# Kernel optimization log

Measured on AMD Instinct MI355X. Metric: run time of the kernel, lower is better.

## Reference

```python
import jax, jax.numpy as jnp
import numpy as np

TOPK_FRAC = 0.05  # init arg `topk` (fraction of pool kept)


def setup_inputs() -> dict:
    key = jax.random.key(0)
    k1, k2 = jax.random.split(key)
    x = jax.random.normal(k1, (16, 256, 32, 32), dtype=jnp.float32)
    # nn.Parameter(torch.rand(P, C)) -> uniform [0, 1)
    visual_concept_pool = jax.random.uniform(k2, (2048, 256), dtype=jnp.float32)
    return {"x": x, "visual_concept_pool": visual_concept_pool}


def reference(x, visual_concept_pool):
    n, c, h, w = x.shape
    P = visual_concept_pool.shape[0]
    L = h * w
    xf = x.reshape(n, c, L)                              # [n, c, L]
    # dot_product[n, P, L] = pool @ xf
    dot = jnp.einsum('pc,ncl->npl', visual_concept_pool, xf)
    pool_norm = jnp.sqrt(jnp.sum(visual_concept_pool ** 2, axis=1))   # [P]
    x_norm = jnp.sqrt(jnp.sum(xf ** 2, axis=1))                        # [n, L]
    cos = dot / (pool_norm[None, :, None] * x_norm[:, None, :])       # [n, P, L]

    # mode 1.1: top-k over the pool dimension per (n, pixel)
    keep = int(TOPK_FRAC * P)
    cos_t = jnp.transpose(cos, (0, 2, 1))                # [n, L, P]
    _, idx = jax.lax.top_k(jnp.abs(cos_t), keep)         # [n, L, keep]
    mask = jnp.zeros_like(cos_t).at[
        jnp.arange(n)[:, None, None],
        jnp.arange(L)[None, :, None],
        idx,
    ].set(1.0)                                           # [n, L, P]
    masked = cos_t * mask
    normed = masked / jnp.sum(masked, axis=-1, keepdims=True)  # renormalize over P
    # reconstruct[n, c, L] = pool^T @ cos
    recon = jnp.einsum('pc,nlp->ncl', visual_concept_pool, normed)
    return recon.reshape(n, c, h, w)
```

## Files before the change

### kernel.cpp

```cpp
#include <hip/hip_runtime.h>
#include <hip/hip_fp16.h>

typedef unsigned short u16;
typedef _Float16 half8 __attribute__((ext_vector_type(8)));
typedef float floatx4 __attribute__((ext_vector_type(4)));

#define C_DIM 256
#define P_DIM 2048
#define L_DIM 1024
#define N_DIM 16
#define KEEP 102
#define KPAD 104
#define QTR_PIX 4096
#define SCALE 256.0f

__device__ __forceinline__ void st8(u16* dst, const u16* s) {
  uint4 u;
  u.x = (unsigned)s[0] | ((unsigned)s[1] << 16);
  u.y = (unsigned)s[2] | ((unsigned)s[3] << 16);
  u.z = (unsigned)s[4] | ((unsigned)s[5] << 16);
  u.w = (unsigned)s[6] | ((unsigned)s[7] << 16);
  *(uint4*)dst = u;
}

__device__ __forceinline__ u16 f2h_ftz(float v) {
  if (fabsf(v) < 6.103515625e-5f) return 0;
  return __half_as_ushort(__float2half(v));
}

__device__ __forceinline__ void gl_lds16(const u16* g, u16* l) {
  __builtin_amdgcn_global_load_lds(
      (const __attribute__((address_space(1))) unsigned int*)g,
      (__attribute__((address_space(3))) unsigned int*)l, 16, 0, 0);
}

union SMem {
  u16 sB[2][2][8][512];
  struct { float tbuf[8][260]; int2 kpw[8][KPAD]; } sel;
};

__global__ __launch_bounds__(256) void k_pinv(const float* __restrict__ pool,
                                              float* __restrict__ pinv) {
  int p = blockIdx.x * 256 + threadIdx.x;
  const float4* row = (const float4*)(pool + (size_t)p * C_DIM);
  float s = 0.f;
#pragma unroll
  for (int i = 0; i < C_DIM / 4; ++i) {
    float4 v = row[i];
    s += v.x * v.x + v.y * v.y + v.z * v.z + v.w * v.w;
  }
  pinv[p] = 1.0f / sqrtf(s);
}

__global__ __launch_bounds__(256) void k_packpool(const float* __restrict__ pool,
                                                  const float* __restrict__ pinv,
                                                  u16* __restrict__ ah,
                                                  u16* __restrict__ al,
                                                  u16* __restrict__ ph) {
  int tid = blockIdx.x * 256 + threadIdx.x;
  int lane = tid & 63;
  int ks = (tid >> 6) & 7;
  int pm = tid >> 9;
  int p = pm * 16 + (lane & 15);
  int c0 = ks * 32 + ((lane >> 4) << 3);
  float sc = pinv[p] * SCALE;
  const float* src = pool + (size_t)p * C_DIM + c0;
  u16 h8[8], l8[8], p8[8];
#pragma unroll
  for (int j = 0; j < 8; ++j) {
    float raw = src[j];
    p8[j] = __half_as_ushort(__float2half(raw));
    float v = raw * sc;
    u16 h = f2h_ftz(v);
    float r = v - __half2float(__ushort_as_half(h));
    h8[j] = h;
    l8[j] = f2h_ftz(r);
  }
  size_t o = (size_t)tid * 8;
  st8(ah + o, h8); st8(al + o, l8);
  st8(ph + (size_t)p * C_DIM + c0, p8);
}

__global__ __launch_bounds__(256) void k_packx(const float* __restrict__ x,
                                               u16* __restrict__ xh,
                                               u16* __restrict__ xl) {
  int tid = blockIdx.x * 256 + threadIdx.x;
  int lane = tid & 63;
  int ks = (tid >> 6) & 7;
  int pn = tid >> 9;
  int pix = pn * 16 + (lane & 15);
  int n = pix >> 10, l = pix & 1023;
  int c0 = ks * 32 + ((lane >> 4) << 3);
  const float* src = x + ((size_t)(n * C_DIM + c0)) * L_DIM + l;
  u16 h8[8], l8[8];
#pragma unroll
  for (int j = 0; j < 8; ++j) {
    float v = src[(size_t)j * L_DIM] * SCALE;
    u16 h = f2h_ftz(v);
    float r = v - __half2float(__ushort_as_half(h));
    h8[j] = h;
    l8[j] = f2h_ftz(r);
  }
  size_t o = (size_t)tid * 8;
  st8(xh + o, h8); st8(xl + o, l8);
}

__device__ __forceinline__ void mfma_body(int b, int mq,
                                          const u16* __restrict__ ah_,
                                          const u16* __restrict__ al_,
                                          const u16* __restrict__ xh_,
                                          const u16* __restrict__ xl_,
                                          float* __restrict__ sbuf,
                                          u16 (*sB)[2][8][512]) {
  const int t = threadIdx.x, lane = t & 63, w = t >> 6;
  const int pT = b & 15, pixT = b >> 4;
  const int pm = pT * 8 + w;
  const int pnBase = mq * 256 + pixT * 8;
  const half8* A8h = (const half8*)ah_;
  const half8* A8l = (const half8*)al_;
  const u16* xsrc[2] = {xh_, xl_};

  floatx4 acc[8];
#pragma unroll
  for (int nt = 0; nt < 8; ++nt) acc[nt] = (floatx4){0.f, 0.f, 0.f, 0.f};

#pragma unroll
  for (int q = 0; q < 2; ++q) {
    int id = w * 2 + q;
    int arr = id >> 3, nt = id & 7;
    gl_lds16(xsrc[arr] + ((size_t)(pnBase + nt) * 512 + lane) * 8,
             &sB[0][arr][nt][0]);
  }
  __syncthreads();

#pragma unroll 1
  for (int ks = 0; ks < 8; ++ks) {
    const int cur = ks & 1;
    half8 aH, aL;
    {
      size_t idx = (size_t)pm * 512 + (size_t)ks * 64 + lane;
      aH = A8h[idx]; aL = A8l[idx];
    }
    if (ks < 7) {
#pragma unroll
      for (int q = 0; q < 2; ++q) {
        int id = w * 2 + q;
        int arr = id >> 3, nt = id & 7;
        gl_lds16(xsrc[arr] + ((size_t)(pnBase + nt) * 512 + (ks + 1) * 64 + lane) * 8,
                 &sB[cur ^ 1][arr][nt][0]);
      }
    }
#pragma unroll
    for (int nt = 0; nt < 8; ++nt) {
      half8 bh = *(const half8*)&sB[cur][0][nt][lane * 8];
      half8 bl = *(const half8*)&sB[cur][1][nt][lane * 8];
      floatx4 c = acc[nt];
      c = __builtin_amdgcn_mfma_f32_16x16x32_f16(aH, bh, c, 0, 0, 0);
      c = __builtin_amdgcn_mfma_f32_16x16x32_f16(aH, bl, c, 0, 0, 0);
      c = __builtin_amdgcn_mfma_f32_16x16x32_f16(aL, bh, c, 0, 0, 0);
      acc[nt] = c;
    }
    __syncthreads();
  }

  const int qr = lane >> 4, cl = lane & 15;
  const int pix0 = pixT * 128;
  const int pcol = pT * 128 + w * 16;
#pragma unroll
  for (int nt = 0; nt < 8; ++nt) {
    float* dst = sbuf + (size_t)(pix0 + nt * 16 + cl) * P_DIM + pcol + qr * 4;
    *(float4*)dst = make_float4(acc[nt][0], acc[nt][1], acc[nt][2], acc[nt][3]);
  }
}

__device__ __forceinline__ void select_body(int b, int sq,
                                            const float* __restrict__ sbuf,
                                            const u16* __restrict__ pool_h,
                                            float* __restrict__ out,
                                            float (*tbuf)[260],
                                            int2 (*kpw)[KPAD]) {
  const int t = threadIdx.x;
  const int lane = t & 63;
  const int wv = t >> 6;
  const int gp0 = sq * QTR_PIX + b * 8;
  const int n = gp0 >> 10;
  const int l0 = gp0 & 1023;
  const float* sp = sbuf + (size_t)(b * 8 + wv) * P_DIM;

  float4 v[8];
#pragma unroll
  for (int q = 0; q < 8; ++q) v[q] = *(const float4*)(sp + q * 256 + lane * 4);

  if (lane < KPAD - KEEP) kpw[wv][KEEP + lane] = make_int2(0, 0);

  float M = 0.f;
#pragma unroll
  for (int q = 0; q < 8; ++q) {
    M = fmaxf(M, fabsf(v[q].x)); M = fmaxf(M, fabsf(v[q].y));
    M = fmaxf(M, fabsf(v[q].z)); M = fmaxf(M, fabsf(v[q].w));
  }
#pragma unroll
  for (int off = 1; off < 64; off <<= 1) M = fmaxf(M, __shfl_xor(M, off));
  const unsigned bitsM = __float_as_uint(M);

  unsigned lo = 0u, hi = bitsM + 1u;
  unsigned m = (bitsM > (5u << 23)) ? (bitsM - (5u << 23)) : ((lo + hi) >> 1);
  while (hi - lo > 1u) {
    float mf = __uint_as_float(m);
    unsigned cnt = 0;
#pragma unroll
    for (int q = 0; q < 8; ++q) {
      cnt += (unsigned)__popcll(__ballot(fabsf(v[q].x) >= mf));
      cnt += (unsigned)__popcll(__ballot(fabsf(v[q].y) >= mf));
      cnt += (unsigned)__popcll(__ballot(fabsf(v[q].z) >= mf));
      cnt += (unsigned)__popcll(__ballot(fabsf(v[q].w) >= mf));
    }
    if (cnt >= KEEP) lo = m; else hi = m;
    m = lo + ((hi - lo) >> 1);
  }
  const float V = __uint_as_float(lo);
  const float Vp = __uint_as_float(lo + 1u);

  unsigned gt = 0;
#pragma unroll
  for (int q = 0; q < 8; ++q) {
    gt += (unsigned)__popcll(__ballot(fabsf(v[q].x) >= Vp));
    gt += (unsigned)__popcll(__ballot(fabsf(v[q].y) >= Vp));
    gt += (unsigned)__popcll(__ballot(fabsf(v[q].z) >= Vp));
    gt += (unsigned)__popcll(__ballot(fabsf(v[q].w) >= Vp));
  }
  const unsigned rrem = (unsigned)KEEP - gt;

  unsigned gmask[8], tmask[8];
#pragma unroll
  for (int q = 0; q < 8; ++q) {
    const float* f = (const float*)&v[q];
    unsigned gm = 0, tm = 0;
#pragma unroll
    for (int rr = 0; rr < 4; ++rr) {
      float av = fabsf(f[rr]);
      if (av >= Vp) gm |= (1u << rr);
      else if (av >= V) tm |= (1u << rr);
    }
    gmask[q] = gm; tmask[q] = tm;
  }

  const unsigned long long lowm = (1ull << lane) - 1ull;
  unsigned base = 0, tiebase = 0;
  float Ssum = 0.f;
#pragma unroll
  for (int q = 0; q < 8; ++q) {
    const float* f = (const float*)&v[q];
    unsigned teq = 0, myeqb = 0;
#pragma unroll
    for (int rr = 0; rr < 4; ++rr) {
      unsigned long long beq = __ballot((tmask[q] >> rr) & 1u);
      teq += (unsigned)__popcll(beq);
      myeqb += (unsigned)__popcll(beq & lowm);
    }
    unsigned km = gmask[q];
    {
      unsigned cum = 0;
#pragma unroll
      for (int rr = 0; rr < 4; ++rr) {
        if ((tmask[q] >> rr) & 1u) {
          if (tiebase + myeqb + cum < rrem) km |= (1u << rr);
          ++cum;
        }
      }
    }
    unsigned long long bk[4];
    unsigned tot = 0, myb = 0;
#pragma unroll
    for (int rr = 0; rr < 4; ++rr) {
      bk[rr] = __ballot((km >> rr) & 1u);
      tot += (unsigned)__popcll(bk[rr]);
      myb += (unsigned)__popcll(bk[rr] & lowm);
    }
    {
      unsigned cum = 0;
#pragma unroll
      for (int rr = 0; rr < 4; ++rr) {
        if ((km >> rr) & 1u) {
          unsigned pos = base + myb + cum;
          kpw[wv][pos] = make_int2(q * 256 + lane * 4 + rr, __float_as_int(f[rr]));
          Ssum += f[rr];
          ++cum;
        }
      }
    }
    base += tot;
    tiebase += teq;
  }

#pragma unroll
  for (int off = 1; off < 64; off <<= 1) Ssum += __shfl_xor(Ssum, off);
  const float invS = 1.0f / Ssum;

  __builtin_amdgcn_wave_barrier();

  float a0 = 0.f, a1 = 0.f, a2 = 0.f, a3 = 0.f;
  const u16* pb = pool_h + 4 * lane;
  int2 e[4];
  uint2 r[4];
#pragma unroll
  for (int j = 0; j < 4; ++j) e[j] = kpw[wv][j];
#pragma unroll
  for (int j = 0; j < 4; ++j) r[j] = *(const uint2*)(pb + (size_t)e[j].x * C_DIM);
  for (int k = 0; k < KPAD; k += 4) {
    int kn = (k + 4 < KPAD) ? k + 4 : 0;
    int2 en[4];
    uint2 rn[4];
#pragma unroll
    for (int j = 0; j < 4; ++j) en[j] = kpw[wv][kn + j];
#pragma unroll
    for (int j = 0; j < 4; ++j) rn[j] = *(const uint2*)(pb + (size_t)en[j].x * C_DIM);
#pragma unroll
    for (int j = 0; j < 4; ++j) {
      float w2 = __int_as_float(e[j].y);
      unsigned rx = r[j].x, ry = r[j].y;
      asm volatile("v_fma_mix_f32 %0, %1, %2, %0 op_sel:[0,0,0] op_sel_hi:[0,1,0]"
                   : "+v"(a0) : "v"(w2), "v"(rx));
      asm volatile("v_fma_mix_f32 %0, %1, %2, %0 op_sel:[0,1,0] op_sel_hi:[0,1,0]"
                   : "+v"(a1) : "v"(w2), "v"(rx));
      asm volatile("v_fma_mix_f32 %0, %1, %2, %0 op_sel:[0,0,0] op_sel_hi:[0,1,0]"
                   : "+v"(a2) : "v"(w2), "v"(ry));
      asm volatile("v_fma_mix_f32 %0, %1, %2, %0 op_sel:[0,1,0] op_sel_hi:[0,1,0]"
                   : "+v"(a3) : "v"(w2), "v"(ry));
    }
#pragma unroll
    for (int j = 0; j < 4; ++j) { e[j] = en[j]; r[j] = rn[j]; }
  }
  a0 *= invS; a1 *= invS; a2 *= invS; a3 *= invS;

  *(float4*)&tbuf[wv][4 * lane] = make_float4(a0, a1, a2, a3);
  __syncthreads();

  {
    int c = t >> 1, lq = t & 1;
    float4 o = make_float4(tbuf[4 * lq + 0][c], tbuf[4 * lq + 1][c],
                           tbuf[4 * lq + 2][c], tbuf[4 * lq + 3][c]);
    *(float4*)(out + ((size_t)(n * C_DIM + c)) * L_DIM + l0 + 4 * lq) = o;
  }
}

__global__ __launch_bounds__(512, 4) void k_main(const u16* __restrict__ ah_,
                                                 const u16* __restrict__ al_,
                                                 const u16* __restrict__ xh_,
                                                 const u16* __restrict__ xl_,
                                                 const u16* __restrict__ ph,
                                                 float* __restrict__ sbuf0,
                                                 float* __restrict__ sbuf1,
                                                 float* __restrict__ out,
                                                 int mq, int sq) {
  __shared__ __align__(16) SMem sm;
  const int b = blockIdx.x;
  const int nsel = (sq >= 0) ? 512 : 0;
  if (b < nsel) {
    select_body(b, sq, (sq & 1) ? sbuf1 : sbuf0, ph, out, sm.sel.tbuf, sm.sel.kpw);
  } else {
    mfma_body(b - nsel, mq, ah_, al_, xh_, xl_, (mq & 1) ? sbuf1 : sbuf0, sm.sB);
  }
}

extern "C" void kernel_launch(void* const* d_in, const int* in_sizes, int n_in,
                              void* d_out, int out_size, void* d_ws, size_t ws_size,
                              hipStream_t stream) {
  const float* x = (const float*)d_in[0];
  const float* pool = (const float*)d_in[1];
  float* out = (float*)d_out;
  char* wsb = (char*)d_ws;
  float* sbuf0 = (float*)wsb;
  float* sbuf1 = (float*)(wsb + 33554432);
  u16* xh = (u16*)(wsb + 67108864);
  u16* xl = xh + 4194304;
  u16* ah = xl + 4194304;
  u16* al = ah + 524288;
  u16* ph = al + 524288;
  float* pinv = (float*)(ph + 524288);

  k_pinv<<<P_DIM / 256, 256, 0, stream>>>(pool, pinv);
  k_packpool<<<256, 256, 0, stream>>>(pool, pinv, ah, al, ph);
  k_packx<<<2048, 256, 0, stream>>>(x, xh, xl);

  k_main<<<512, 512, 0, stream>>>(ah, al, xh, xl, ph, sbuf0, sbuf1, out, 0, -1);
  k_main<<<1024, 512, 0, stream>>>(ah, al, xh, xl, ph, sbuf0, sbuf1, out, 1, 0);
  k_main<<<1024, 512, 0, stream>>>(ah, al, xh, xl, ph, sbuf0, sbuf1, out, 2, 1);
  k_main<<<1024, 512, 0, stream>>>(ah, al, xh, xl, ph, sbuf0, sbuf1, out, 3, 2);
  k_main<<<512, 512, 0, stream>>>(ah, al, xh, xl, ph, sbuf0, sbuf1, out, -1, 3);
}
```

Before: 270.1 us.

## Overlap x packing with MFMA quarters and speed up top-k threshold search

Merges the pool and first-quarter x packing into one pre-kernel. The remaining x quarters are packed inside k_main launches so they run alongside the previous quarter's MFMA and select work, hiding conversion cost and removing launches. The top-k threshold bisection now alternates interpolation steps with halving and exits early on an exact count, which skips the tie-handling ballots when no ties remain. The risks are extra branching, and wave divergence if interpolation does not converge faster than bisection.

```diff
diff --git a/kernel.cpp b/kernel.cpp
--- a/kernel.cpp
+++ b/kernel.cpp
@@ -52,12 +52,13 @@
   pinv[p] = 1.0f / sqrtf(s);
 }
 
-__global__ __launch_bounds__(256) void k_packpool(const float* __restrict__ pool,
-                                                  const float* __restrict__ pinv,
-                                                  u16* __restrict__ ah,
-                                                  u16* __restrict__ al,
-                                                  u16* __restrict__ ph) {
-  int tid = blockIdx.x * 256 + threadIdx.x;
+__device__ __forceinline__ void packpool_body(int b,
+                                              const float* __restrict__ pool,
+                                              const float* __restrict__ pinv,
+                                              u16* __restrict__ ah,
+                                              u16* __restrict__ al,
+                                              u16* __restrict__ ph) {
+  int tid = b * 512 + threadIdx.x;
   int lane = tid & 63;
   int ks = (tid >> 6) & 7;
   int pm = tid >> 9;
@@ -81,13 +82,14 @@
   st8(ph + (size_t)p * C_DIM + c0, p8);
 }
 
-__global__ __launch_bounds__(256) void k_packx(const float* __restrict__ x,
-                                               u16* __restrict__ xh,
-                                               u16* __restrict__ xl) {
-  int tid = blockIdx.x * 256 + threadIdx.x;
-  int lane = tid & 63;
-  int ks = (tid >> 6) & 7;
-  int pn = tid >> 9;
+__device__ __forceinline__ void packx_body(int pb, int pq,
+                                           const float* __restrict__ x,
+                                           u16* __restrict__ xh,
+                                           u16* __restrict__ xl) {
+  int t = threadIdx.x;
+  int lane = t & 63;
+  int ks = (t >> 6) & 7;
+  int pn = pq * 256 + pb;
   int pix = pn * 16 + (lane & 15);
   int n = pix >> 10, l = pix & 1023;
   int c0 = ks * 32 + ((lane >> 4) << 3);
@@ -101,8 +103,21 @@
     h8[j] = h;
     l8[j] = f2h_ftz(r);
   }
-  size_t o = (size_t)tid * 8;
+  size_t o = ((size_t)pn * 512 + (size_t)ks * 64 + lane) * 8;
   st8(xh + o, h8); st8(xl + o, l8);
+}
+
+__global__ __launch_bounds__(512) void k_pre(const float* __restrict__ pool,
+                                             const float* __restrict__ pinv,
+                                             u16* __restrict__ ah,
+                                             u16* __restrict__ al,
+                                             u16* __restrict__ ph,
+                                             const float* __restrict__ x,
+                                             u16* __restrict__ xh,
+                                             u16* __restrict__ xl) {
+  int b = blockIdx.x;
+  if (b < 128) packpool_body(b, pool, pinv, ah, al, ph);
+  else packx_body(b - 128, 0, x, xh, xl);
 }
 
 __device__ __forceinline__ void mfma_body(int b, int mq,
@@ -204,7 +219,10 @@
   const unsigned bitsM = __float_as_uint(M);
 
   unsigned lo = 0u, hi = bitsM + 1u;
+  unsigned cl = 2048u, ch = 0u;
+  bool exact = false;
   unsigned m = (bitsM > (5u << 23)) ? (bitsM - (5u << 23)) : ((lo + hi) >> 1);
+  int it = 0;
   while (hi - lo > 1u) {
     float mf = __uint_as_float(m);
     unsigned cnt = 0;
@@ -215,21 +233,35 @@
       cnt += (unsigned)__popcll(__ballot(fabsf(v[q].z) >= mf));
       cnt += (unsigned)__popcll(__ballot(fabsf(v[q].w) >= mf));
     }
-    if (cnt >= KEEP) lo = m; else hi = m;
-    m = lo + ((hi - lo) >> 1);
+    if (cnt == (unsigned)KEEP) { lo = m; exact = true; break; }
+    if (cnt > (unsigned)KEEP) { lo = m; cl = cnt; } else { hi = m; ch = cnt; }
+    unsigned span = hi - lo;
+    if (span <= 1u) break;
+    unsigned step;
+    if ((++it & 1) != 0) {
+      step = (unsigned)((float)span * (float)(cl - KEEP) / (float)(cl - ch));
+    } else {
+      step = span >> 1;
+    }
+    if (step < 1u) step = 1u;
+    else if (step > span - 1u) step = span - 1u;
+    m = lo + step;
   }
   const float V = __uint_as_float(lo);
-  const float Vp = __uint_as_float(lo + 1u);
-
-  unsigned gt = 0;
-#pragma unroll
-  for (int q = 0; q < 8; ++q) {
-    gt += (unsigned)__popcll(__ballot(fabsf(v[q].x) >= Vp));
-    gt += (unsigned)__popcll(__ballot(fabsf(v[q].y) >= Vp));
-    gt += (unsigned)__popcll(__ballot(fabsf(v[q].z) >= Vp));
-    gt += (unsigned)__popcll(__ballot(fabsf(v[q].w) >= Vp));
-  }
-  const unsigned rrem = (unsigned)KEEP - gt;
+  const float Vp = exact ? V : __uint_as_float(lo + 1u);
+
+  unsigned rrem = 0u;
+  if (!exact) {
+    unsigned gt = 0;
+#pragma unroll
+    for (int q = 0; q < 8; ++q) {
+      gt += (unsigned)__popcll(__ballot(fabsf(v[q].x) >= Vp));
+      gt += (unsigned)__popcll(__ballot(fabsf(v[q].y) >= Vp));
+      gt += (unsigned)__popcll(__ballot(fabsf(v[q].z) >= Vp));
+      gt += (unsigned)__popcll(__ballot(fabsf(v[q].w) >= Vp));
+    }
+    rrem = (unsigned)KEEP - gt;
+  }
 
   unsigned gmask[8], tmask[8];
 #pragma unroll
@@ -251,15 +283,15 @@
 #pragma unroll
   for (int q = 0; q < 8; ++q) {
     const float* f = (const float*)&v[q];
-    unsigned teq = 0, myeqb = 0;
-#pragma unroll
-    for (int rr = 0; rr < 4; ++rr) {
-      unsigned long long beq = __ballot((tmask[q] >> rr) & 1u);
-      teq += (unsigned)__popcll(beq);
-      myeqb += (unsigned)__popcll(beq & lowm);
-    }
     unsigned km = gmask[q];
-    {
+    if (rrem != 0u) {
+      unsigned teq = 0, myeqb = 0;
+#pragma unroll
+      for (int rr = 0; rr < 4; ++rr) {
+        unsigned long long beq = __ballot((tmask[q] >> rr) & 1u);
+        teq += (unsigned)__popcll(beq);
+        myeqb += (unsigned)__popcll(beq & lowm);
+      }
       unsigned cum = 0;
 #pragma unroll
       for (int rr = 0; rr < 4; ++rr) {
@@ -268,6 +300,7 @@
           ++cum;
         }
       }
+      tiebase += teq;
     }
     unsigned long long bk[4];
     unsigned tot = 0, myb = 0;
@@ -290,7 +323,6 @@
       }
     }
     base += tot;
-    tiebase += teq;
   }
 
 #pragma unroll
@@ -349,17 +381,21 @@
                                                  const u16* __restrict__ xh_,
                                                  const u16* __restrict__ xl_,
                                                  const u16* __restrict__ ph,
+                                                 const float* __restrict__ x,
                                                  float* __restrict__ sbuf0,
                                                  float* __restrict__ sbuf1,
                                                  float* __restrict__ out,
-                                                 int mq, int sq) {
+                                                 int mq, int sq, int pq) {
   __shared__ __align__(16) SMem sm;
   const int b = blockIdx.x;
   const int nsel = (sq >= 0) ? 512 : 0;
+  const int npk = (pq >= 0) ? 256 : 0;
   if (b < nsel) {
     select_body(b, sq, (sq & 1) ? sbuf1 : sbuf0, ph, out, sm.sel.tbuf, sm.sel.kpw);
+  } else if (b < nsel + npk) {
+    packx_body(b - nsel, pq, x, (u16*)xh_, (u16*)xl_);
   } else {
-    mfma_body(b - nsel, mq, ah_, al_, xh_, xl_, (mq & 1) ? sbuf1 : sbuf0, sm.sB);
+    mfma_body(b - nsel - npk, mq, ah_, al_, xh_, xl_, (mq & 1) ? sbuf1 : sbuf0, sm.sB);
   }
 }
 
@@ -380,12 +416,11 @@
   float* pinv = (float*)(ph + 524288);
 
   k_pinv<<<P_DIM / 256, 256, 0, stream>>>(pool, pinv);
-  k_packpool<<<256, 256, 0, stream>>>(pool, pinv, ah, al, ph);
-  k_packx<<<2048, 256, 0, stream>>>(x, xh, xl);
-
-  k_main<<<512, 512, 0, stream>>>(ah, al, xh, xl, ph, sbuf0, sbuf1, out, 0, -1);
-  k_main<<<1024, 512, 0, stream>>>(ah, al, xh, xl, ph, sbuf0, sbuf1, out, 1, 0);
-  k_main<<<1024, 512, 0, stream>>>(ah, al, xh, xl, ph, sbuf0, sbuf1, out, 2, 1);
-  k_main<<<1024, 512, 0, stream>>>(ah, al, xh, xl, ph, sbuf0, sbuf1, out, 3, 2);
-  k_main<<<512, 512, 0, stream>>>(ah, al, xh, xl, ph, sbuf0, sbuf1, out, -1, 3);
-}
+  k_pre<<<384, 512, 0, stream>>>(pool, pinv, ah, al, ph, x, xh, xl);
+
+  k_main<<<768, 512, 0, stream>>>(ah, al, xh, xl, ph, x, sbuf0, sbuf1, out, 0, -1, 1);
+  k_main<<<1280, 512, 0, stream>>>(ah, al, xh, xl, ph, x, sbuf0, sbuf1, out, 1, 0, 2);
+  k_main<<<1280, 512, 0, stream>>>(ah, al, xh, xl, ph, x, sbuf0, sbuf1, out, 2, 1, 3);
+  k_main<<<1024, 512, 0, stream>>>(ah, al, xh, xl, ph, x, sbuf0, sbuf1, out, 3, 2, -1);
+  k_main<<<512, 512, 0, stream>>>(ah, al, xh, xl, ph, x, sbuf0, sbuf1, out, -1, 3, -1);
+}
```

After: 252.7 us. -6.4%, faster.
